# Performance work log

Hardware: AMD Instinct MI355X
Metric: run time of the kernel (lower is better)

The kernel has to match this reference:

```python
import jax, jax.numpy as jnp
import numpy as np

H = 128          # hidden_dim
EPS = 1e-5       # BatchNorm eps


def _mean_aggr(h_src, src_idx, dst_idx, num_dst):
    # scatter-mean of h_src rows (gathered by src_idx) onto dst nodes
    msgs = h_src[src_idx]                                   # [E, H] gather
    s = jax.ops.segment_sum(msgs, dst_idx, num_segments=num_dst)
    c = jax.ops.segment_sum(jnp.ones((dst_idx.shape[0],), h_src.dtype),
                            dst_idx, num_segments=num_dst)
    return s / jnp.maximum(c, 1.0)[:, None]


def _bn_eval(h, g, b, m, v):
    return (h - m) * jax.lax.rsqrt(v + EPS) * g + b


def setup_inputs() -> dict:
    key = jax.random.key(0)
    ks = jax.random.split(key, 32)
    Nu, Nr, E, Din, ED = 100000, 100000, 500000, 32, 16
    d = {}
    d['x_user'] = jax.random.normal(ks[0], (Nu, Din), jnp.float32)
    d['x_recipient'] = jax.random.normal(ks[1], (Nr, Din), jnp.float32)
    d['edge_attr'] = jax.random.normal(ks[2], (E, ED), jnp.float32)
    d['edge_index_ut'] = jax.random.randint(ks[3], (2, E), 0, Nr)  # user->recipient
    d['edge_index_ru'] = jax.random.randint(ks[4], (2, E), 0, Nu)  # recipient->user
    sc = 0.05
    # input projections (Linear: y = x @ W + b, W stored [in, out])
    d['proj_uW'] = jax.random.normal(ks[5], (Din, H), jnp.float32) * sc
    d['proj_ub'] = jnp.zeros((H,), jnp.float32)
    d['proj_rW'] = jax.random.normal(ks[6], (Din, H), jnp.float32) * sc
    d['proj_rb'] = jnp.zeros((H,), jnp.float32)
    # SAGEConv params: [num_layers=2, num_edge_types=2, ...]
    d['sage_Wl'] = jax.random.normal(ks[7], (2, 2, H, H), jnp.float32) * sc
    d['sage_bl'] = jnp.zeros((2, 2, H), jnp.float32)
    d['sage_Wr'] = jax.random.normal(ks[8], (2, 2, H, H), jnp.float32) * sc
    # BatchNorm (eval): [num_layers=2, num_node_types=2 (0=user,1=recipient), H]
    d['bn_g'] = jnp.ones((2, 2, H), jnp.float32)
    d['bn_b'] = jnp.zeros((2, 2, H), jnp.float32)
    d['bn_m'] = jax.random.normal(ks[9], (2, 2, H), jnp.float32) * 0.01
    d['bn_v'] = jnp.ones((2, 2, H), jnp.float32)
    # EdgePredictor MLP: (2H + edge_dim) -> H -> H//2 -> 1
    din = 2 * H + ED
    d['ep_W1'] = jax.random.normal(ks[10], (din, H), jnp.float32) * sc
    d['ep_b1'] = jnp.zeros((H,), jnp.float32)
    d['ep_bng'] = jnp.ones((H,), jnp.float32)
    d['ep_bnb'] = jnp.zeros((H,), jnp.float32)
    d['ep_bnm'] = jax.random.normal(ks[11], (H,), jnp.float32) * 0.01
    d['ep_bnv'] = jnp.ones((H,), jnp.float32)
    d['ep_W2'] = jax.random.normal(ks[12], (H, H // 2), jnp.float32) * sc
    d['ep_b2'] = jnp.zeros((H // 2,), jnp.float32)
    d['ep_W3'] = jax.random.normal(ks[13], (H // 2, 1), jnp.float32) * sc
    d['ep_b3'] = jnp.zeros((1,), jnp.float32)
    return d


def reference(x_user, x_recipient, edge_attr, edge_index_ut, edge_index_ru,
              proj_uW, proj_ub, proj_rW, proj_rb,
              sage_Wl, sage_bl, sage_Wr,
              bn_g, bn_b, bn_m, bn_v,
              ep_W1, ep_b1, ep_bng, ep_bnb, ep_bnm, ep_bnv,
              ep_W2, ep_b2, ep_W3, ep_b3):
    Nu = x_user.shape[0]
    Nr = x_recipient.shape[0]
    # input projections
    h_u = x_user @ proj_uW + proj_ub        # [Nu, H]
    h_r = x_recipient @ proj_rW + proj_rb   # [Nr, H]

    for i in range(2):  # num_layers
        # edge type 0: user -> recipient (SAGE mean aggr + root)
        agg_r = _mean_aggr(h_u, edge_index_ut[0], edge_index_ut[1], Nr)
        new_r = agg_r @ sage_Wl[i, 0] + sage_bl[i, 0] + h_r @ sage_Wr[i, 0]
        # edge type 1: recipient -> user
        agg_u = _mean_aggr(h_r, edge_index_ru[0], edge_index_ru[1], Nu)
        new_u = agg_u @ sage_Wl[i, 1] + sage_bl[i, 1] + h_u @ sage_Wr[i, 1]
        # BN (eval) + ReLU (dropout inactive) + residual
        new_u = jax.nn.relu(_bn_eval(new_u, bn_g[i, 0], bn_b[i, 0], bn_m[i, 0], bn_v[i, 0])) + h_u
        new_r = jax.nn.relu(_bn_eval(new_r, bn_g[i, 1], bn_b[i, 1], bn_m[i, 1], bn_v[i, 1])) + h_r
        h_u, h_r = new_u, new_r

    # edge predictor on target edge type (user -> recipient)
    src = h_u[edge_index_ut[0]]   # [E, H]
    dst = h_r[edge_index_ut[1]]   # [E, H]
    x = jnp.concatenate([src, dst, edge_attr], axis=1)  # [E, 2H+ED]
    h = jax.nn.relu(x @ ep_W1 + ep_b1)
    h = _bn_eval(h, ep_bng, ep_bnb, ep_bnm, ep_bnv)
    h = jax.nn.relu(h @ ep_W2 + ep_b2)
    out = jax.nn.sigmoid(h @ ep_W3 + ep_b3)
    return out.squeeze(-1)  # [E]
```

## Files before the change

### kernel.cpp

```cpp
#include <hip/hip_runtime.h>
#include <math.h>

#define H 128
#define BN_EPS 1e-5f

typedef __attribute__((ext_vector_type(8))) short bf16x8;
typedef __attribute__((ext_vector_type(4))) float f32x4;

__device__ __forceinline__ unsigned short f2bf(float f) {
    unsigned int u = __float_as_uint(f);
    u += 0x7fffu + ((u >> 16) & 1u);
    return (unsigned short)(u >> 16);
}
__device__ __forceinline__ float bf2f(unsigned short s) {
    return __uint_as_float(((unsigned int)s) << 16);
}
__device__ __forceinline__ f32x4 mfma16(bf16x8 a, bf16x8 b, f32x4 c) {
    return __builtin_amdgcn_mfma_f32_16x16x32_bf16(a, b, c, 0, 0, 0);
}

__device__ __forceinline__ void wfrag_one(const float* __restrict__ src,
                                          unsigned short* __restrict__ dst,
                                          int K, int N, int idx) {
    int l = idx & 63;
    int rest = idx >> 6;
    int ntn = N >> 4;
    int nt = rest % ntn;
    int kc = rest / ntn;
    int n = nt * 16 + (l & 15);
    int k0 = kc * 32 + (l >> 4) * 8;
    bf16x8 v;
    #pragma unroll
    for (int j = 0; j < 8; ++j) {
        int k = k0 + j;
        v[j] = (short)((k < K) ? f2bf(src[(size_t)k * N + n]) : 0);
    }
    *(bf16x8*)(dst + (size_t)idx * 8) = v;
}

__global__ __launch_bounds__(256)
void wfrag_all(const float* __restrict__ W1, const float* __restrict__ W2,
               const float* __restrict__ pu, const float* __restrict__ pr,
               const float* __restrict__ Wl, const float* __restrict__ Wr,
               unsigned short* __restrict__ W1f, unsigned short* __restrict__ W2f,
               unsigned short* __restrict__ puf, unsigned short* __restrict__ prf,
               unsigned short* __restrict__ sageWf) {
    int bx = blockIdx.x;
    if (bx < 26) {
        int idx = bx * 256 + threadIdx.x;
        if (idx < 4608)      wfrag_one(W1, W1f, 272, 128, idx);
        else if (idx < 5632) wfrag_one(W2, W2f, 128, 64, idx - 4608);
        else if (idx < 6144) wfrag_one(pu, puf, 32, 128, idx - 5632);
        else if (idx < 6656) wfrag_one(pr, prf, 32, 128, idx - 6144);
    } else {
        int idx = (bx - 26) * 256 + threadIdx.x;
        int seg = idx >> 11;
        int sub = idx & 2047;
        int lt = seg >> 1;
        int half = seg & 1;
        const float* src = (half ? Wr : Wl) + (size_t)lt * H * H;
        unsigned short* dst = sageWf + (size_t)lt * 32768 + half * 16384;
        wfrag_one(src, dst, 128, 128, sub);
    }
}

__global__ __launch_bounds__(256)
void proj_kernel(const float* __restrict__ xu, const float* __restrict__ xr,
                 const unsigned short* __restrict__ puf, const float* __restrict__ bu,
                 const unsigned short* __restrict__ prf, const float* __restrict__ br,
                 unsigned short* __restrict__ hub, unsigned short* __restrict__ hrb,
                 int Nu, int Nr, int nbu) {
    int bx = blockIdx.x;
    const float* x; const unsigned short* Wf; const float* bias;
    unsigned short* hb; int N; int row0;
    if (bx < nbu) { x = xu; Wf = puf; bias = bu; hb = hub; N = Nu; row0 = bx * 64; }
    else          { x = xr; Wf = prf; bias = br; hb = hrb; N = Nr; row0 = (bx - nbu) * 64; }

    int tid = threadIdx.x, l = tid & 63, w = tid >> 6, l15 = l & 15, quad = l >> 4;
    int arow = row0 + w * 16 + l15;

    bf16x8 a = {0, 0, 0, 0, 0, 0, 0, 0};
    if (arow < N) {
        const float* xp = x + (size_t)arow * 32 + quad * 8;
        float4 v0 = *(const float4*)xp;
        float4 v1 = *(const float4*)(xp + 4);
        a[0] = (short)f2bf(v0.x); a[1] = (short)f2bf(v0.y);
        a[2] = (short)f2bf(v0.z); a[3] = (short)f2bf(v0.w);
        a[4] = (short)f2bf(v1.x); a[5] = (short)f2bf(v1.y);
        a[6] = (short)f2bf(v1.z); a[7] = (short)f2bf(v1.w);
    }
    f32x4 acc[8];
    #pragma unroll
    for (int nt = 0; nt < 8; ++nt) {
        bf16x8 b = *(const bf16x8*)(Wf + (size_t)(nt * 64 + l) * 8);
        acc[nt] = mfma16(a, b, (f32x4){0.f, 0.f, 0.f, 0.f});
    }
    #pragma unroll
    for (int reg = 0; reg < 4; ++reg) {
        int row = row0 + w * 16 + quad * 4 + reg;
        if (row < N) {
            #pragma unroll
            for (int nt = 0; nt < 8; ++nt) {
                int col = nt * 16 + l15;
                hb[(size_t)row * H + col] = f2bf(acc[nt][reg] + bias[col]);
            }
        }
    }
}

__global__ __launch_bounds__(256)
void hist_kernel(const int* __restrict__ dstR, const int* __restrict__ dstU,
                 int* __restrict__ degR, int* __restrict__ degU, int E, int EB) {
    int bx = blockIdx.x;
    const int* dst = (bx < EB) ? dstR : dstU;
    int* deg = (bx < EB) ? degR : degU;
    int e = ((bx < EB) ? bx : bx - EB) * 256 + threadIdx.x;
    if (e < E) atomicAdd(&deg[dst[e]], 1);
}

__global__ __launch_bounds__(256)
void scan1_kernel(const int* __restrict__ degR, const int* __restrict__ degU,
                  int* __restrict__ partR, int* __restrict__ partU, int Nr, int Nu, int NBr) {
    int bx = blockIdx.x;
    const int* deg = (bx < NBr) ? degR : degU;
    int* part = (bx < NBr) ? partR : partU;
    int lb = (bx < NBr) ? bx : bx - NBr;
    int N = (bx < NBr) ? Nr : Nu;
    __shared__ int s[256];
    int t = threadIdx.x;
    int i = lb * 256 + t;
    s[t] = (i < N) ? deg[i] : 0;
    __syncthreads();
    for (int o = 128; o > 0; o >>= 1) {
        if (t < o) s[t] += s[t + o];
        __syncthreads();
    }
    if (t == 0) part[lb] = s[0];
}

__global__ __launch_bounds__(512)
void scan2_kernel(int* __restrict__ partR, int* __restrict__ partU, int nbR, int nbU) {
    int* part = (blockIdx.x == 0) ? partR : partU;
    int nb = (blockIdx.x == 0) ? nbR : nbU;
    __shared__ int s[512];
    int t = threadIdx.x;
    int v = (t < nb) ? part[t] : 0;
    s[t] = v;
    __syncthreads();
    for (int o = 1; o < 512; o <<= 1) {
        int x = (t >= o) ? s[t - o] : 0;
        __syncthreads();
        s[t] += x;
        __syncthreads();
    }
    if (t < nb) part[t] = s[t] - v;
}

__global__ __launch_bounds__(256)
void scan3_kernel(const int* __restrict__ degR, const int* __restrict__ degU,
                  const int* __restrict__ partR, const int* __restrict__ partU,
                  int* __restrict__ offR, int* __restrict__ offU, int Nr, int Nu, int NBr) {
    int bx = blockIdx.x;
    const int* deg = (bx < NBr) ? degR : degU;
    const int* part = (bx < NBr) ? partR : partU;
    int* off = (bx < NBr) ? offR : offU;
    int lb = (bx < NBr) ? bx : bx - NBr;
    int N = (bx < NBr) ? Nr : Nu;
    __shared__ int s[256];
    int t = threadIdx.x;
    int i = lb * 256 + t;
    int v = (i < N) ? deg[i] : 0;
    s[t] = v;
    __syncthreads();
    for (int o = 1; o < 256; o <<= 1) {
        int x = (t >= o) ? s[t - o] : 0;
        __syncthreads();
        s[t] += x;
        __syncthreads();
    }
    if (i < N) off[i] = part[lb] + s[t] - v;
    if (i == N - 1) off[N] = part[lb] + s[t];
}

__global__ __launch_bounds__(256)
void fill_kernel(const int* __restrict__ srcR, const int* __restrict__ dstR,
                 const int* __restrict__ srcU, const int* __restrict__ dstU,
                 const int* __restrict__ offR, const int* __restrict__ offU,
                 int* __restrict__ degR, int* __restrict__ degU,
                 int* __restrict__ eidR, int* __restrict__ eidU,
                 int* __restrict__ epermR, int* __restrict__ epdstR,
                 int E, int EB) {
    int bx = blockIdx.x;
    bool isR = bx < EB;
    const int* src = isR ? srcR : srcU;
    const int* dst = isR ? dstR : dstU;
    const int* off = isR ? offR : offU;
    int* deg = isR ? degR : degU;
    int* eid = isR ? eidR : eidU;
    int e = (isR ? bx : bx - EB) * 256 + threadIdx.x;
    if (e < E) {
        int d = dst[e];
        int p = off[d] + atomicSub(&deg[d], 1) - 1;
        eid[p] = src[e];
        if (isR) {
            epermR[p] = e;
            epdstR[p] = d;
        }
    }
}

__global__ __launch_bounds__(256)
void layer_kernel(const unsigned short* __restrict__ hu_o, const unsigned short* __restrict__ hr_o,
                  unsigned short* __restrict__ hu_n, unsigned short* __restrict__ hr_n,
                  const int* __restrict__ off_r, const int* __restrict__ eid_r,
                  const int* __restrict__ off_u, const int* __restrict__ eid_u,
                  int Nu, int Nr, int nbr,
                  const unsigned short* __restrict__ WfR, const float* __restrict__ blR,
                  const float* __restrict__ gR, const float* __restrict__ bR,
                  const float* __restrict__ mR, const float* __restrict__ vR,
                  const unsigned short* __restrict__ WfU, const float* __restrict__ blU,
                  const float* __restrict__ gU, const float* __restrict__ bU,
                  const float* __restrict__ mU, const float* __restrict__ vU) {
    int bx = blockIdx.x;
    const unsigned short* gsrc; const unsigned short* own; unsigned short* outp;
    const int* off; const int* eid; const unsigned short* Wf;
    const float *bl, *bg, *bb, *bm, *bv;
    int N, row0;
    if (bx < nbr) {
        gsrc = hu_o; own = hr_o; outp = hr_n; off = off_r; eid = eid_r;
        Wf = WfR; bl = blR; bg = gR; bb = bR; bm = mR; bv = vR;
        N = Nr; row0 = bx * 64;
    } else {
        gsrc = hr_o; own = hu_o; outp = hu_n; off = off_u; eid = eid_u;
        Wf = WfU; bl = blU; bg = gU; bb = bU; bm = mU; bv = vU;
        N = Nu; row0 = (bx - nbr) * 64;
    }

    __shared__ float sc[128], sh[128], bias[128];
    int tid = threadIdx.x;
    if (tid < 128) {
        float s = bg[tid] * rsqrtf(bv[tid] + BN_EPS);
        sc[tid] = s;
        sh[tid] = bb[tid] - bm[tid] * s;
        bias[tid] = bl[tid];
    }
    __syncthreads();

    int l = tid & 63, w = tid >> 6, l15 = l & 15, quad = l >> 4;
    int arow = row0 + w * 16 + l15;
    bool rok = (arow < N);
    size_t rbase = (size_t)(rok ? arow : 0) * H;
    int s0 = rok ? off[arow] : 0;
    int s1 = rok ? off[arow + 1] : 0;

    bf16x8 ownfr[4];
    #pragma unroll
    for (int kc = 0; kc < 4; ++kc)
        ownfr[kc] = *(const bf16x8*)(own + rbase + kc * 32 + quad * 8);

    float ag[4][8];
    #pragma unroll
    for (int kc = 0; kc < 4; ++kc)
        #pragma unroll
        for (int j = 0; j < 8; ++j) ag[kc][j] = 0.0f;

    for (int i = s0; i < s1; ++i) {
        int s = eid[i];
        const unsigned short* rp = gsrc + (size_t)s * H + quad * 8;
        #pragma unroll
        for (int kc = 0; kc < 4; ++kc) {
            bf16x8 v = *(const bf16x8*)(rp + kc * 32);
            #pragma unroll
            for (int j = 0; j < 8; ++j) ag[kc][j] += bf2f((unsigned short)v[j]);
        }
    }
    float inv = (s1 > s0) ? 1.0f / (float)(s1 - s0) : 0.0f;

    f32x4 acc[8];
    #pragma unroll
    for (int nt = 0; nt < 8; ++nt) acc[nt] = (f32x4){0.f, 0.f, 0.f, 0.f};

    #pragma unroll
    for (int kc = 0; kc < 4; ++kc) {
        bf16x8 a;
        #pragma unroll
        for (int j = 0; j < 8; ++j) a[j] = (short)f2bf(ag[kc][j] * inv);
        #pragma unroll
        for (int nt = 0; nt < 8; ++nt) {
            bf16x8 b = *(const bf16x8*)(Wf + (size_t)((kc * 8 + nt) * 64 + l) * 8);
            acc[nt] = mfma16(a, b, acc[nt]);
        }
    }
    #pragma unroll
    for (int kc = 4; kc < 8; ++kc) {
        #pragma unroll
        for (int nt = 0; nt < 8; ++nt) {
            bf16x8 b = *(const bf16x8*)(Wf + (size_t)((kc * 8 + nt) * 64 + l) * 8);
            acc[nt] = mfma16(ownfr[kc - 4], b, acc[nt]);
        }
    }

    #pragma unroll
    for (int reg = 0; reg < 4; ++reg) {
        int crow = row0 + w * 16 + quad * 4 + reg;
        if (crow < N) {
            #pragma unroll
            for (int nt = 0; nt < 8; ++nt) {
                int col = nt * 16 + l15;
                float g = acc[nt][reg] + bias[col];
                g = g * sc[col] + sh[col];
                float hv = bf2f(own[(size_t)crow * H + col]);
                outp[(size_t)crow * H + col] = f2bf(fmaxf(g, 0.0f) + hv);
            }
        }
    }
}

__global__ __launch_bounds__(256)
void ep_kernel(const unsigned short* __restrict__ hub, const unsigned short* __restrict__ hrb,
               const float* __restrict__ ea,
               const int* __restrict__ slot_src, const int* __restrict__ slot_dst,
               const int* __restrict__ slot_eid,
               const unsigned short* __restrict__ W1f, const float* __restrict__ b1,
               const float* __restrict__ bng, const float* __restrict__ bnb,
               const float* __restrict__ bnm, const float* __restrict__ bnv,
               const unsigned short* __restrict__ W2f, const float* __restrict__ b2,
               const float* __restrict__ W3, const float* __restrict__ b3,
               float* __restrict__ out, int E) {
    __shared__ unsigned short h1s[64][136];
    __shared__ int se[64], de[64], pe[64];
    __shared__ float sc1[128], sh1[128], bi1[128];

    int tid = threadIdx.x;
    int p0 = blockIdx.x * 64;
    if (tid < 64) {
        int p = p0 + tid;
        bool v = (p < E);
        se[tid] = v ? slot_src[p] : 0;
        de[tid] = v ? slot_dst[p] : 0;
        pe[tid] = v ? slot_eid[p] : 0;
    }
    if (tid < 128) {
        float s = bng[tid] * rsqrtf(bnv[tid] + BN_EPS);
        sc1[tid] = s;
        sh1[tid] = bnb[tid] - bnm[tid] * s;
        bi1[tid] = b1[tid];
    }
    __syncthreads();

    int l = tid & 63, w = tid >> 6, l15 = l & 15, quad = l >> 4;
    int arow = w * 16 + l15;
    size_t soff = (size_t)se[arow] * H;
    size_t doff = (size_t)de[arow] * H;
    int eorig = pe[arow];
    bool ev = (p0 + arow < E);

    bf16x8 afr[9];
    #pragma unroll
    for (int kc = 0; kc < 4; ++kc)
        afr[kc] = *(const bf16x8*)(hub + soff + kc * 32 + quad * 8);
    #pragma unroll
    for (int kc = 0; kc < 4; ++kc)
        afr[4 + kc] = *(const bf16x8*)(hrb + doff + kc * 32 + quad * 8);
    {
        bf16x8 a = {0, 0, 0, 0, 0, 0, 0, 0};
        if (quad < 2 && ev) {
            const float* p = ea + (size_t)eorig * 16 + quad * 8;
            float4 v0 = *(const float4*)p;
            float4 v1 = *(const float4*)(p + 4);
            a[0] = (short)f2bf(v0.x); a[1] = (short)f2bf(v0.y);
            a[2] = (short)f2bf(v0.z); a[3] = (short)f2bf(v0.w);
            a[4] = (short)f2bf(v1.x); a[5] = (short)f2bf(v1.y);
            a[6] = (short)f2bf(v1.z); a[7] = (short)f2bf(v1.w);
        }
        afr[8] = a;
    }

    f32x4 acc[8];
    #pragma unroll
    for (int nt = 0; nt < 8; ++nt) acc[nt] = (f32x4){0.f, 0.f, 0.f, 0.f};

    #pragma unroll
    for (int kc = 0; kc < 9; ++kc) {
        #pragma unroll
        for (int nt = 0; nt < 8; ++nt) {
            bf16x8 b = *(const bf16x8*)(W1f + (size_t)((kc * 8 + nt) * 64 + l) * 8);
            acc[nt] = mfma16(afr[kc], b, acc[nt]);
        }
    }

    #pragma unroll
    for (int nt = 0; nt < 8; ++nt) {
        #pragma unroll
        for (int reg = 0; reg < 4; ++reg) {
            int row = w * 16 + quad * 4 + reg;
            int col = nt * 16 + l15;
            float z = acc[nt][reg] + bi1[col];
            z = fmaxf(z, 0.0f);
            z = z * sc1[col] + sh1[col];
            h1s[row][col] = f2bf(z);
        }
    }
    __syncthreads();

    f32x4 acc2[4];
    #pragma unroll
    for (int nt = 0; nt < 4; ++nt) acc2[nt] = (f32x4){0.f, 0.f, 0.f, 0.f};
    #pragma unroll
    for (int kc = 0; kc < 4; ++kc) {
        bf16x8 a2 = *(const bf16x8*)&h1s[w * 16 + l15][kc * 32 + quad * 8];
        #pragma unroll
        for (int nt = 0; nt < 4; ++nt) {
            bf16x8 b = *(const bf16x8*)(W2f + (size_t)((kc * 4 + nt) * 64 + l) * 8);
            acc2[nt] = mfma16(a2, b, acc2[nt]);
        }
    }

    float part[4] = {0.f, 0.f, 0.f, 0.f};
    #pragma unroll
    for (int nt = 0; nt < 4; ++nt) {
        int col = nt * 16 + l15;
        float w3v = W3[col];
        float b2v = b2[col];
        #pragma unroll
        for (int reg = 0; reg < 4; ++reg)
            part[reg] += fmaxf(acc2[nt][reg] + b2v, 0.0f) * w3v;
    }
    #pragma unroll
    for (int m = 1; m < 16; m <<= 1) {
        #pragma unroll
        for (int reg = 0; reg < 4; ++reg)
            part[reg] += __shfl_xor(part[reg], m);
    }
    if (l15 < 4) {
        int row = w * 16 + quad * 4 + l15;
        if (p0 + row < E) {
            int eo = pe[row];
            out[eo] = 1.0f / (1.0f + expf(-(part[l15] + b3[0])));
        }
    }
}

extern "C" void kernel_launch(void* const* d_in, const int* in_sizes, int n_in,
                              void* d_out, int out_size, void* d_ws, size_t ws_size,
                              hipStream_t stream) {
    const float* x_u     = (const float*)d_in[0];
    const float* x_r     = (const float*)d_in[1];
    const float* eattr   = (const float*)d_in[2];
    const int*   ei_ut   = (const int*)d_in[3];
    const int*   ei_ru   = (const int*)d_in[4];
    const float* proj_uW = (const float*)d_in[5];
    const float* proj_ub = (const float*)d_in[6];
    const float* proj_rW = (const float*)d_in[7];
    const float* proj_rb = (const float*)d_in[8];
    const float* sage_Wl = (const float*)d_in[9];
    const float* sage_bl = (const float*)d_in[10];
    const float* sage_Wr = (const float*)d_in[11];
    const float* bn_g    = (const float*)d_in[12];
    const float* bn_b    = (const float*)d_in[13];
    const float* bn_m    = (const float*)d_in[14];
    const float* bn_v    = (const float*)d_in[15];
    const float* ep_W1   = (const float*)d_in[16];
    const float* ep_b1   = (const float*)d_in[17];
    const float* ep_bng  = (const float*)d_in[18];
    const float* ep_bnb  = (const float*)d_in[19];
    const float* ep_bnm  = (const float*)d_in[20];
    const float* ep_bnv  = (const float*)d_in[21];
    const float* ep_W2   = (const float*)d_in[22];
    const float* ep_b2   = (const float*)d_in[23];
    const float* ep_W3   = (const float*)d_in[24];
    const float* ep_b3   = (const float*)d_in[25];

    int Nu = in_sizes[0] / 32;
    int Nr = in_sizes[1] / 32;
    int E  = in_sizes[3] / 2;

    unsigned short* us = (unsigned short*)d_ws;
    unsigned short* h0_u = us;   us += (size_t)Nu * H;
    unsigned short* h0_r = us;   us += (size_t)Nr * H;
    unsigned short* h1_u = us;   us += (size_t)Nu * H;
    unsigned short* h1_r = us;   us += (size_t)Nr * H;
    unsigned short* W1f  = us;   us += 36864;
    unsigned short* W2f  = us;   us += 8192;
    unsigned short* puf  = us;   us += 4096;
    unsigned short* prf  = us;   us += 4096;
    unsigned short* sageWf = us; us += 131072;
    int* ip     = (int*)us;
    int* off_r  = ip;  ip += Nr + 1;
    int* off_u  = ip;  ip += Nu + 1;
    int* deg_r  = ip;  ip += Nr;
    int* deg_u  = ip;  ip += Nu;
    int* eid_r  = ip;  ip += E;
    int* eid_u  = ip;  ip += E;
    int* eperm_r = ip; ip += E;
    int* epdst_r = ip; ip += E;
    int* part_r = ip;  ip += 512;
    int* part_u = ip;  ip += 512;

    const int* ut_src = ei_ut;
    const int* ut_dst = ei_ut + E;
    const int* ru_src = ei_ru;
    const int* ru_dst = ei_ru + E;

    int EB  = (E + 255) / 256;
    int NBr = (Nr + 255) / 256;
    int NBu = (Nu + 255) / 256;

    wfrag_all<<<90, 256, 0, stream>>>(ep_W1, ep_W2, proj_uW, proj_rW,
                                      sage_Wl, sage_Wr,
                                      W1f, W2f, puf, prf, sageWf);

    hipMemsetAsync(deg_r, 0, (size_t)(Nr + Nu) * sizeof(int), stream);
    hist_kernel<<<2 * EB, 256, 0, stream>>>(ut_dst, ru_dst, deg_r, deg_u, E, EB);
    scan1_kernel<<<NBr + NBu, 256, 0, stream>>>(deg_r, deg_u, part_r, part_u, Nr, Nu, NBr);
    scan2_kernel<<<2, 512, 0, stream>>>(part_r, part_u, NBr, NBu);
    scan3_kernel<<<NBr + NBu, 256, 0, stream>>>(deg_r, deg_u, part_r, part_u,
                                                off_r, off_u, Nr, Nu, NBr);
    fill_kernel<<<2 * EB, 256, 0, stream>>>(ut_src, ut_dst, ru_src, ru_dst,
                                            off_r, off_u, deg_r, deg_u,
                                            eid_r, eid_u, eperm_r, epdst_r, E, EB);

    int nbu = (Nu + 63) / 64, nbr = (Nr + 63) / 64;
    proj_kernel<<<nbu + nbr, 256, 0, stream>>>(x_u, x_r, puf, proj_ub, prf, proj_rb,
                                               h0_u, h0_r, Nu, Nr, nbu);

    for (int layer = 0; layer < 2; ++layer) {
        const unsigned short* iu = (layer == 0) ? h0_u : h1_u;
        const unsigned short* ir = (layer == 0) ? h0_r : h1_r;
        unsigned short* ou = (layer == 0) ? h1_u : h0_u;
        unsigned short* orr = (layer == 0) ? h1_r : h0_r;

        const unsigned short* Wf0 = sageWf + ((size_t)layer * 2 + 0) * 32768;
        const unsigned short* Wf1 = sageWf + ((size_t)layer * 2 + 1) * 32768;
        const float* bl0 = sage_bl + ((size_t)layer * 2 + 0) * H;
        const float* bl1 = sage_bl + ((size_t)layer * 2 + 1) * H;
        const float* g0 = bn_g + ((size_t)layer * 2 + 0) * H;
        const float* b0 = bn_b + ((size_t)layer * 2 + 0) * H;
        const float* m0 = bn_m + ((size_t)layer * 2 + 0) * H;
        const float* v0 = bn_v + ((size_t)layer * 2 + 0) * H;
        const float* g1 = bn_g + ((size_t)layer * 2 + 1) * H;
        const float* b1 = bn_b + ((size_t)layer * 2 + 1) * H;
        const float* m1 = bn_m + ((size_t)layer * 2 + 1) * H;
        const float* v1 = bn_v + ((size_t)layer * 2 + 1) * H;

        layer_kernel<<<nbr + nbu, 256, 0, stream>>>(
            iu, ir, ou, orr,
            off_r, eid_r, off_u, eid_u,
            Nu, Nr, nbr,
            Wf0, bl0, g1, b1, m1, v1,
            Wf1, bl1, g0, b0, m0, v0);
    }

    ep_kernel<<<(E + 63) / 64, 256, 0, stream>>>(h0_u, h0_r, eattr,
                                                 eid_r, epdst_r, eperm_r,
                                                 W1f, ep_b1,
                                                 ep_bng, ep_bnb, ep_bnm, ep_bnv,
                                                 W2f, ep_b2, ep_W3, ep_b3,
                                                 (float*)d_out, E);
}
```

Measured before the change: 578.8 us.

## Sort rows by degree within SAGE tiles and fold block-prefix scan into scan3

Removes the separate scan2 launch. Each scan3 block now reduces the raw per-block partial sums before its own block to get its prefix offset. In the SAGE layer kernel, the 64 rows of each tile are bitonic-sorted by in-degree with wave shuffles and processed in that order. Lanes in a 16-row MFMA group then have similar gather loop lengths, which cuts divergence, at the cost of a small sort and indirect row indexing.

```diff
diff --git a/kernel.cpp b/kernel.cpp
--- a/kernel.cpp
+++ b/kernel.cpp
@@ -138,24 +138,6 @@
     if (t == 0) part[lb] = s[0];
 }
 
-__global__ __launch_bounds__(512)
-void scan2_kernel(int* __restrict__ partR, int* __restrict__ partU, int nbR, int nbU) {
-    int* part = (blockIdx.x == 0) ? partR : partU;
-    int nb = (blockIdx.x == 0) ? nbR : nbU;
-    __shared__ int s[512];
-    int t = threadIdx.x;
-    int v = (t < nb) ? part[t] : 0;
-    s[t] = v;
-    __syncthreads();
-    for (int o = 1; o < 512; o <<= 1) {
-        int x = (t >= o) ? s[t - o] : 0;
-        __syncthreads();
-        s[t] += x;
-        __syncthreads();
-    }
-    if (t < nb) part[t] = s[t] - v;
-}
-
 __global__ __launch_bounds__(256)
 void scan3_kernel(const int* __restrict__ degR, const int* __restrict__ degU,
                   const int* __restrict__ partR, const int* __restrict__ partU,
@@ -167,7 +149,20 @@
     int lb = (bx < NBr) ? bx : bx - NBr;
     int N = (bx < NBr) ? Nr : Nu;
     __shared__ int s[256];
+    __shared__ int ps[256];
     int t = threadIdx.x;
+
+    int pv = 0;
+    if (t < lb) pv += part[t];
+    if (t + 256 < lb) pv += part[t + 256];
+    ps[t] = pv;
+    __syncthreads();
+    for (int o = 128; o > 0; o >>= 1) {
+        if (t < o) ps[t] += ps[t + o];
+        __syncthreads();
+    }
+    int pref = ps[0];
+
     int i = lb * 256 + t;
     int v = (i < N) ? deg[i] : 0;
     s[t] = v;
@@ -178,8 +173,8 @@
         s[t] += x;
         __syncthreads();
     }
-    if (i < N) off[i] = part[lb] + s[t] - v;
-    if (i == N - 1) off[N] = part[lb] + s[t];
+    if (i < N) off[i] = pref + s[t] - v;
+    if (i == N - 1) off[N] = pref + s[t];
 }
 
 __global__ __launch_bounds__(256)
@@ -237,6 +232,7 @@
     }
 
     __shared__ float sc[128], sh[128], bias[128];
+    __shared__ int perm[64];
     int tid = threadIdx.x;
     if (tid < 128) {
         float s = bg[tid] * rsqrtf(bv[tid] + BN_EPS);
@@ -244,10 +240,24 @@
         sh[tid] = bb[tid] - bm[tid] * s;
         bias[tid] = bl[tid];
     }
+    if (tid < 64) {
+        int rr = row0 + tid;
+        int dg = (rr < N) ? (off[rr + 1] - off[rr]) : 0;
+        int key = (min(dg, 255) << 8) | tid;
+        for (int k = 2; k <= 64; k <<= 1) {
+            for (int j = k >> 1; j > 0; j >>= 1) {
+                int p = __shfl_xor(key, j);
+                bool keepmin = (((tid & j) == 0) == ((tid & k) == 0));
+                key = keepmin ? (key < p ? key : p) : (key > p ? key : p);
+            }
+        }
+        perm[tid] = key & 255;
+    }
     __syncthreads();
 
     int l = tid & 63, w = tid >> 6, l15 = l & 15, quad = l >> 4;
-    int arow = row0 + w * 16 + l15;
+    int rloc = perm[w * 16 + l15];
+    int arow = row0 + rloc;
     bool rok = (arow < N);
     size_t rbase = (size_t)(rok ? arow : 0) * H;
     int s0 = rok ? off[arow] : 0;
@@ -302,7 +312,7 @@
 
     #pragma unroll
     for (int reg = 0; reg < 4; ++reg) {
-        int crow = row0 + w * 16 + quad * 4 + reg;
+        int crow = row0 + perm[w * 16 + quad * 4 + reg];
         if (crow < N) {
             #pragma unroll
             for (int nt = 0; nt < 8; ++nt) {
@@ -513,7 +523,6 @@
     hipMemsetAsync(deg_r, 0, (size_t)(Nr + Nu) * sizeof(int), stream);
     hist_kernel<<<2 * EB, 256, 0, stream>>>(ut_dst, ru_dst, deg_r, deg_u, E, EB);
     scan1_kernel<<<NBr + NBu, 256, 0, stream>>>(deg_r, deg_u, part_r, part_u, Nr, Nu, NBr);
-    scan2_kernel<<<2, 512, 0, stream>>>(part_r, part_u, NBr, NBu);
     scan3_kernel<<<NBr + NBu, 256, 0, stream>>>(deg_r, deg_u, part_r, part_u,
                                                 off_r, off_u, Nr, Nu, NBr);
     fill_kernel<<<2 * EB, 256, 0, stream>>>(ut_src, ut_dst, ru_src, ru_dst,
```

Result: faster. 553.8 us (-4.3%).
